# Kernel optimization log

Measured on AMD Instinct MI355X. Metric: run time of the kernel, lower is better.

Reference implementation:

```python
import jax, jax.numpy as jnp
import numpy as np

N_THRESHOLDS = 10


def setup_inputs() -> dict:
    key = jax.random.key(0)
    k1, k2, k3 = jax.random.split(key, 3)
    shape = (32, 1024, 1024)
    prediction = jax.random.normal(k1, shape, dtype=jnp.float32)
    mask = jax.random.randint(k2, shape, 0, 2, dtype=jnp.int32)
    target = jax.random.randint(k3, shape, 0, 2, dtype=jnp.int32)
    return {"prediction": prediction, "mask": mask, "target": target}


def reference(prediction, mask, target):
    # thresholds = linspace(0,1,n+2)[1:-1], same as the torch module
    thresholds = jnp.linspace(0.0, 1.0, N_THRESHOLDS + 2, dtype=jnp.float32)[1:-1]

    s = jax.nn.sigmoid(prediction).ravel()            # [N]
    m = mask.ravel().astype(bool)                     # [N] valid mask
    t = target.ravel().astype(bool)                   # [N]
    mt = m & t                                        # masked positives

    # Broadcast compare against all thresholds at once (single fused pass,
    # no per-threshold host sync like the original loop).
    pos = s[None, :] > thresholds[:, None]            # [T, N] bool

    tp = jnp.sum(pos & mt[None, :], axis=1)           # [T] int32
    p = jnp.sum(pos & m[None, :], axis=1)             # predicted-positive count

    total_m = jnp.sum(m)                              # total valid elements
    total_t = jnp.sum(mt)                             # total true positives in mask

    fp = p - tp
    fn = total_t - tp
    tn = total_m - p - fn

    # classes layout matches torch module: rows = [tp, fp, tn, fn]
    return jnp.stack([tp, fp, tn, fn], axis=0).astype(jnp.float32)
```

## Files before the change

### kernel.cpp

```cpp
#include <hip/hip_runtime.h>


#define NTHR 10
#define NBKT 11
#define NCNT 22
#define WS_STRIDE 16

typedef unsigned long long u64;
typedef unsigned u32;
typedef float __attribute__((ext_vector_type(4))) f32x4;
typedef int   __attribute__((ext_vector_type(4))) i32x4;

__device__ __forceinline__ unsigned wave_reduce_add(unsigned v) {
#pragma unroll
    for (int off = 32; off > 0; off >>= 1)
        v += __shfl_down(v, off, 64);
    return v;
}

__global__ __launch_bounds__(64) void zero_ws_kernel(u32* __restrict__ ws) {
    int i = threadIdx.x;
    if (i < NCNT) ws[i * WS_STRIDE] = 0u;
}

__device__ __forceinline__ void acc_elem(float x, u32 mm, u32 tt, u64& hP, u64& hT) {
    u32 mt = mm & tt;
    float e = __expf(-x);
    float s = __builtin_amdgcn_rcpf(1.0f + e);
    int bi = (int)(s * 11.0f);
    u32 b = (u32)(bi > 10 ? 10 : bi);
    u32 sh = b * 5u;
    hP += (u64)mm << sh;
    hT += (u64)mt << sh;
}

__device__ __forceinline__ void acc_vec(const f32x4& p, const i32x4& m, const i32x4& t,
                                        u64& hP, u64& hT) {
    acc_elem(p.x, (u32)m.x, (u32)t.x, hP, hT);
    acc_elem(p.y, (u32)m.y, (u32)t.y, hP, hT);
    acc_elem(p.z, (u32)m.z, (u32)t.z, hP, hT);
    acc_elem(p.w, (u32)m.w, (u32)t.w, hP, hT);
}

__device__ __forceinline__ void flush_hist(u64& hP, u64& hT,
                                           u64& Plo, u64& Phi, u64& Tlo, u64& Thi) {
#pragma unroll
    for (int b = 0; b < 6; ++b) {
        Plo += (u64)((u32)(hP >> (5 * b)) & 31u) << (10 * b);
        Tlo += (u64)((u32)(hT >> (5 * b)) & 31u) << (10 * b);
    }
#pragma unroll
    for (int b = 6; b < NBKT; ++b) {
        Phi += (u64)((u32)(hP >> (5 * b)) & 31u) << (10 * (b - 6));
        Thi += (u64)((u32)(hT >> (5 * b)) & 31u) << (10 * (b - 6));
    }
    hP = 0ull; hT = 0ull;
}

__global__ __launch_bounds__(256) void count_kernel(
        const f32x4* __restrict__ pred4,
        const i32x4* __restrict__ mask4,
        const i32x4* __restrict__ targ4,
        const float* __restrict__ pred,
        const int*   __restrict__ mask,
        const int*   __restrict__ targ,
        u32* __restrict__ ws, int nvec, int n) {
    u64 Plo = 0ull, Phi = 0ull, Tlo = 0ull, Thi = 0ull;

    const int tid    = blockIdx.x * blockDim.x + threadIdx.x;
    const int lane   = tid & 63;
    const int waveId = tid >> 6;
    const int totalWaves = (gridDim.x * blockDim.x) >> 6;
    const int strideG    = totalWaves << 8;

    for (int base = waveId << 8; base < nvec; base += strideG) {
        u64 hP = 0ull, hT = 0ull;
        if (base + 256 <= nvec) {
            f32x4 p0 = __builtin_nontemporal_load(pred4 + base +       lane);
            f32x4 p1 = __builtin_nontemporal_load(pred4 + base +  64 + lane);
            f32x4 p2 = __builtin_nontemporal_load(pred4 + base + 128 + lane);
            f32x4 p3 = __builtin_nontemporal_load(pred4 + base + 192 + lane);
            i32x4 m0 = __builtin_nontemporal_load(mask4 + base +       lane);
            i32x4 m1 = __builtin_nontemporal_load(mask4 + base +  64 + lane);
            i32x4 m2 = __builtin_nontemporal_load(mask4 + base + 128 + lane);
            i32x4 m3 = __builtin_nontemporal_load(mask4 + base + 192 + lane);
            i32x4 t0 = __builtin_nontemporal_load(targ4 + base +       lane);
            i32x4 t1 = __builtin_nontemporal_load(targ4 + base +  64 + lane);
            i32x4 t2 = __builtin_nontemporal_load(targ4 + base + 128 + lane);
            i32x4 t3 = __builtin_nontemporal_load(targ4 + base + 192 + lane);
            acc_vec(p0, m0, t0, hP, hT);
            acc_vec(p1, m1, t1, hP, hT);
            acc_vec(p2, m2, t2, hP, hT);
            acc_vec(p3, m3, t3, hP, hT);
        } else {
#pragma unroll
            for (int c = 0; c < 4; ++c) {
                int g = base + (c << 6) + lane;
                if (g < nvec) {
                    f32x4 p = __builtin_nontemporal_load(pred4 + g);
                    i32x4 m = __builtin_nontemporal_load(mask4 + g);
                    i32x4 t = __builtin_nontemporal_load(targ4 + g);
                    acc_vec(p, m, t, hP, hT);
                }
            }
        }
        flush_hist(hP, hT, Plo, Phi, Tlo, Thi);
    }

    {
        int i = nvec * 4 + tid;
        if (i < n) {
            u64 hP = 0ull, hT = 0ull;
            acc_elem(pred[i], (u32)mask[i], (u32)targ[i], hP, hT);
            flush_hist(hP, hT, Plo, Phi, Tlo, Thi);
        }
    }

    u32 vals[NCNT];
#pragma unroll
    for (int b = 0; b < 6; ++b) {
        vals[b]        = (u32)(Plo >> (10 * b)) & 1023u;
        vals[NBKT + b] = (u32)(Tlo >> (10 * b)) & 1023u;
    }
#pragma unroll
    for (int b = 6; b < NBKT; ++b) {
        vals[b]        = (u32)(Phi >> (10 * (b - 6))) & 1023u;
        vals[NBKT + b] = (u32)(Thi >> (10 * (b - 6))) & 1023u;
    }
#pragma unroll
    for (int c = 0; c < NCNT; ++c) vals[c] = wave_reduce_add(vals[c]);

    __shared__ u32 partial[4][NCNT];
    const int wave = threadIdx.x >> 6;
    if ((threadIdx.x & 63) == 0) {
#pragma unroll
        for (int c = 0; c < NCNT; ++c) partial[wave][c] = vals[c];
    }
    __syncthreads();
    if (threadIdx.x < NCNT) {
        u32 s = partial[0][threadIdx.x] + partial[1][threadIdx.x] +
                partial[2][threadIdx.x] + partial[3][threadIdx.x];
        atomicAdd(&ws[threadIdx.x * WS_STRIDE], s);
    }
}

__global__ __launch_bounds__(64) void finalize_kernel(const u32* __restrict__ ws,
                                                      float* __restrict__ out) {
    int j = threadIdx.x;
    if (j < NTHR) {
        u32 totM = 0u, totT = 0u, p = 0u, tp = 0u;
#pragma unroll
        for (int b = 0; b < NBKT; ++b) {
            u32 vP = ws[b * WS_STRIDE];
            u32 vT = ws[(NBKT + b) * WS_STRIDE];
            totM += vP; totT += vT;
            if (b > j) { p += vP; tp += vT; }
        }
        u32 fp = p - tp;
        u32 fn = totT - tp;
        u32 tn = totM - p - fn;
        out[j]            = (float)tp;
        out[NTHR + j]     = (float)fp;
        out[2 * NTHR + j] = (float)tn;
        out[3 * NTHR + j] = (float)fn;
    }
}

extern "C" void kernel_launch(void* const* d_in, const int* in_sizes, int n_in,
                              void* d_out, int out_size, void* d_ws, size_t ws_size,
                              hipStream_t stream) {
    const float* pred = (const float*)d_in[0];
    const int*   mask = (const int*)d_in[1];
    const int*   targ = (const int*)d_in[2];
    u32*         ws   = (u32*)d_ws;
    float*       out  = (float*)d_out;

    const int n    = in_sizes[0];
    const int nvec = n / 4;

    zero_ws_kernel<<<1, 64, 0, stream>>>(ws);

    const int blocks = 2048;
    count_kernel<<<blocks, 256, 0, stream>>>(
        (const f32x4*)pred, (const i32x4*)mask, (const i32x4*)targ,
        pred, mask, targ, ws, nvec, n);

    finalize_kernel<<<1, 64, 0, stream>>>(ws, out);
}
```

Before: 332.8 us.

## Double-buffer batch loads in count kernel and halve grid size

```diff
diff --git a/kernel.cpp b/kernel.cpp
--- a/kernel.cpp
+++ b/kernel.cpp
@@ -57,7 +57,66 @@
     hP = 0ull; hT = 0ull;
 }
 
-__global__ __launch_bounds__(256) void count_kernel(
+struct Batch {
+    f32x4 p0, p1, p2, p3;
+    i32x4 m0, m1, m2, m3;
+    i32x4 t0, t1, t2, t3;
+};
+
+__device__ __forceinline__ f32x4 zf4() { f32x4 v; v.x = v.y = v.z = v.w = 0.0f; return v; }
+__device__ __forceinline__ i32x4 zi4() { i32x4 v; v.x = v.y = v.z = v.w = 0;    return v; }
+
+__device__ __forceinline__ void load_batch(Batch& b,
+        const f32x4* __restrict__ pred4, const i32x4* __restrict__ mask4,
+        const i32x4* __restrict__ targ4, int base, int lane, int nvec) {
+    if (base + 256 <= nvec) {
+        b.p0 = __builtin_nontemporal_load(pred4 + base +       lane);
+        b.p1 = __builtin_nontemporal_load(pred4 + base +  64 + lane);
+        b.p2 = __builtin_nontemporal_load(pred4 + base + 128 + lane);
+        b.p3 = __builtin_nontemporal_load(pred4 + base + 192 + lane);
+        b.m0 = __builtin_nontemporal_load(mask4 + base +       lane);
+        b.m1 = __builtin_nontemporal_load(mask4 + base +  64 + lane);
+        b.m2 = __builtin_nontemporal_load(mask4 + base + 128 + lane);
+        b.m3 = __builtin_nontemporal_load(mask4 + base + 192 + lane);
+        b.t0 = __builtin_nontemporal_load(targ4 + base +       lane);
+        b.t1 = __builtin_nontemporal_load(targ4 + base +  64 + lane);
+        b.t2 = __builtin_nontemporal_load(targ4 + base + 128 + lane);
+        b.t3 = __builtin_nontemporal_load(targ4 + base + 192 + lane);
+    } else {
+        int g0 = base +       lane;
+        int g1 = base +  64 + lane;
+        int g2 = base + 128 + lane;
+        int g3 = base + 192 + lane;
+        if (g0 < nvec) { b.p0 = __builtin_nontemporal_load(pred4 + g0);
+                         b.m0 = __builtin_nontemporal_load(mask4 + g0);
+                         b.t0 = __builtin_nontemporal_load(targ4 + g0); }
+        else           { b.p0 = zf4(); b.m0 = zi4(); b.t0 = zi4(); }
+        if (g1 < nvec) { b.p1 = __builtin_nontemporal_load(pred4 + g1);
+                         b.m1 = __builtin_nontemporal_load(mask4 + g1);
+                         b.t1 = __builtin_nontemporal_load(targ4 + g1); }
+        else           { b.p1 = zf4(); b.m1 = zi4(); b.t1 = zi4(); }
+        if (g2 < nvec) { b.p2 = __builtin_nontemporal_load(pred4 + g2);
+                         b.m2 = __builtin_nontemporal_load(mask4 + g2);
+                         b.t2 = __builtin_nontemporal_load(targ4 + g2); }
+        else           { b.p2 = zf4(); b.m2 = zi4(); b.t2 = zi4(); }
+        if (g3 < nvec) { b.p3 = __builtin_nontemporal_load(pred4 + g3);
+                         b.m3 = __builtin_nontemporal_load(mask4 + g3);
+                         b.t3 = __builtin_nontemporal_load(targ4 + g3); }
+        else           { b.p3 = zf4(); b.m3 = zi4(); b.t3 = zi4(); }
+    }
+}
+
+__device__ __forceinline__ void consume_batch(const Batch& b,
+        u64& Plo, u64& Phi, u64& Tlo, u64& Thi) {
+    u64 hP = 0ull, hT = 0ull;
+    acc_vec(b.p0, b.m0, b.t0, hP, hT);
+    acc_vec(b.p1, b.m1, b.t1, hP, hT);
+    acc_vec(b.p2, b.m2, b.t2, hP, hT);
+    acc_vec(b.p3, b.m3, b.t3, hP, hT);
+    flush_hist(hP, hT, Plo, Phi, Tlo, Thi);
+}
+
+__global__ __launch_bounds__(256, 4) void count_kernel(
         const f32x4* __restrict__ pred4,
         const i32x4* __restrict__ mask4,
         const i32x4* __restrict__ targ4,
@@ -73,38 +132,25 @@
     const int totalWaves = (gridDim.x * blockDim.x) >> 6;
     const int strideG    = totalWaves << 8;
 
-    for (int base = waveId << 8; base < nvec; base += strideG) {
-        u64 hP = 0ull, hT = 0ull;
-        if (base + 256 <= nvec) {
-            f32x4 p0 = __builtin_nontemporal_load(pred4 + base +       lane);
-            f32x4 p1 = __builtin_nontemporal_load(pred4 + base +  64 + lane);
-            f32x4 p2 = __builtin_nontemporal_load(pred4 + base + 128 + lane);
-            f32x4 p3 = __builtin_nontemporal_load(pred4 + base + 192 + lane);
-            i32x4 m0 = __builtin_nontemporal_load(mask4 + base +       lane);
-            i32x4 m1 = __builtin_nontemporal_load(mask4 + base +  64 + lane);
-            i32x4 m2 = __builtin_nontemporal_load(mask4 + base + 128 + lane);
-            i32x4 m3 = __builtin_nontemporal_load(mask4 + base + 192 + lane);
-            i32x4 t0 = __builtin_nontemporal_load(targ4 + base +       lane);
-            i32x4 t1 = __builtin_nontemporal_load(targ4 + base +  64 + lane);
-            i32x4 t2 = __builtin_nontemporal_load(targ4 + base + 128 + lane);
-            i32x4 t3 = __builtin_nontemporal_load(targ4 + base + 192 + lane);
-            acc_vec(p0, m0, t0, hP, hT);
-            acc_vec(p1, m1, t1, hP, hT);
-            acc_vec(p2, m2, t2, hP, hT);
-            acc_vec(p3, m3, t3, hP, hT);
-        } else {
-#pragma unroll
-            for (int c = 0; c < 4; ++c) {
-                int g = base + (c << 6) + lane;
-                if (g < nvec) {
-                    f32x4 p = __builtin_nontemporal_load(pred4 + g);
-                    i32x4 m = __builtin_nontemporal_load(mask4 + g);
-                    i32x4 t = __builtin_nontemporal_load(targ4 + g);
-                    acc_vec(p, m, t, hP, hT);
-                }
+    {
+        Batch A, B;
+        int base = waveId << 8;
+        if (base < nvec) {
+            load_batch(A, pred4, mask4, targ4, base, lane, nvec);
+            for (;;) {
+                int nb = base + strideG;
+                if (nb < nvec) load_batch(B, pred4, mask4, targ4, nb, lane, nvec);
+                consume_batch(A, Plo, Phi, Tlo, Thi);
+                if (nb >= nvec) break;
+                base = nb;
+
+                nb = base + strideG;
+                if (nb < nvec) load_batch(A, pred4, mask4, targ4, nb, lane, nvec);
+                consume_batch(B, Plo, Phi, Tlo, Thi);
+                if (nb >= nvec) break;
+                base = nb;
             }
         }
-        flush_hist(hP, hT, Plo, Phi, Tlo, Thi);
     }
 
     {
@@ -180,7 +226,7 @@
 
     zero_ws_kernel<<<1, 64, 0, stream>>>(ws);
 
-    const int blocks = 2048;
+    const int blocks = 1024;
     count_kernel<<<blocks, 256, 0, stream>>>(
         (const f32x4*)pred, (const i32x4*)mask, (const i32x4*)targ,
         pred, mask, targ, ws, nvec, n);
```

New measurement: 422.1 us. 26.8% more time.

## Double-buffer global loads in count kernel and halve grid size

Applied to the files above, without the earlier changes.

```diff
diff --git a/kernel.cpp b/kernel.cpp
--- a/kernel.cpp
+++ b/kernel.cpp
@@ -57,6 +57,56 @@
     hP = 0ull; hT = 0ull;
 }
 
+__device__ __forceinline__ f32x4 zf4() { f32x4 v; v.x = v.y = v.z = v.w = 0.0f; return v; }
+__device__ __forceinline__ i32x4 zi4() { i32x4 v; v.x = v.y = v.z = v.w = 0;    return v; }
+
+#define NTL(p) __builtin_nontemporal_load(p)
+
+#define LOAD_BATCH(S, b)                                                      \
+    do {                                                                      \
+        if ((b) + 256 <= nvec) {                                              \
+            S##p0 = NTL(pred4 + (b) +       lane);                            \
+            S##p1 = NTL(pred4 + (b) +  64 + lane);                            \
+            S##p2 = NTL(pred4 + (b) + 128 + lane);                            \
+            S##p3 = NTL(pred4 + (b) + 192 + lane);                            \
+            S##m0 = NTL(mask4 + (b) +       lane);                            \
+            S##m1 = NTL(mask4 + (b) +  64 + lane);                            \
+            S##m2 = NTL(mask4 + (b) + 128 + lane);                            \
+            S##m3 = NTL(mask4 + (b) + 192 + lane);                            \
+            S##t0 = NTL(targ4 + (b) +       lane);                            \
+            S##t1 = NTL(targ4 + (b) +  64 + lane);                            \
+            S##t2 = NTL(targ4 + (b) + 128 + lane);                            \
+            S##t3 = NTL(targ4 + (b) + 192 + lane);                            \
+        } else {                                                              \
+            int g0 = (b) +       lane;                                        \
+            int g1 = (b) +  64 + lane;                                        \
+            int g2 = (b) + 128 + lane;                                        \
+            int g3 = (b) + 192 + lane;                                        \
+            if (g0 < nvec) { S##p0 = NTL(pred4 + g0); S##m0 = NTL(mask4 + g0);\
+                             S##t0 = NTL(targ4 + g0); }                       \
+            else           { S##p0 = zf4(); S##m0 = zi4(); S##t0 = zi4(); }   \
+            if (g1 < nvec) { S##p1 = NTL(pred4 + g1); S##m1 = NTL(mask4 + g1);\
+                             S##t1 = NTL(targ4 + g1); }                       \
+            else           { S##p1 = zf4(); S##m1 = zi4(); S##t1 = zi4(); }   \
+            if (g2 < nvec) { S##p2 = NTL(pred4 + g2); S##m2 = NTL(mask4 + g2);\
+                             S##t2 = NTL(targ4 + g2); }                       \
+            else           { S##p2 = zf4(); S##m2 = zi4(); S##t2 = zi4(); }   \
+            if (g3 < nvec) { S##p3 = NTL(pred4 + g3); S##m3 = NTL(mask4 + g3);\
+                             S##t3 = NTL(targ4 + g3); }                       \
+            else           { S##p3 = zf4(); S##m3 = zi4(); S##t3 = zi4(); }   \
+        }                                                                     \
+    } while (0)
+
+#define CONSUME_BATCH(S)                                                      \
+    do {                                                                      \
+        u64 hP = 0ull, hT = 0ull;                                             \
+        acc_vec(S##p0, S##m0, S##t0, hP, hT);                                 \
+        acc_vec(S##p1, S##m1, S##t1, hP, hT);                                 \
+        acc_vec(S##p2, S##m2, S##t2, hP, hT);                                 \
+        acc_vec(S##p3, S##m3, S##t3, hP, hT);                                 \
+        flush_hist(hP, hT, Plo, Phi, Tlo, Thi);                               \
+    } while (0)
+
 __global__ __launch_bounds__(256) void count_kernel(
         const f32x4* __restrict__ pred4,
         const i32x4* __restrict__ mask4,
@@ -73,38 +123,30 @@
     const int totalWaves = (gridDim.x * blockDim.x) >> 6;
     const int strideG    = totalWaves << 8;
 
-    for (int base = waveId << 8; base < nvec; base += strideG) {
-        u64 hP = 0ull, hT = 0ull;
-        if (base + 256 <= nvec) {
-            f32x4 p0 = __builtin_nontemporal_load(pred4 + base +       lane);
-            f32x4 p1 = __builtin_nontemporal_load(pred4 + base +  64 + lane);
-            f32x4 p2 = __builtin_nontemporal_load(pred4 + base + 128 + lane);
-            f32x4 p3 = __builtin_nontemporal_load(pred4 + base + 192 + lane);
-            i32x4 m0 = __builtin_nontemporal_load(mask4 + base +       lane);
-            i32x4 m1 = __builtin_nontemporal_load(mask4 + base +  64 + lane);
-            i32x4 m2 = __builtin_nontemporal_load(mask4 + base + 128 + lane);
-            i32x4 m3 = __builtin_nontemporal_load(mask4 + base + 192 + lane);
-            i32x4 t0 = __builtin_nontemporal_load(targ4 + base +       lane);
-            i32x4 t1 = __builtin_nontemporal_load(targ4 + base +  64 + lane);
-            i32x4 t2 = __builtin_nontemporal_load(targ4 + base + 128 + lane);
-            i32x4 t3 = __builtin_nontemporal_load(targ4 + base + 192 + lane);
-            acc_vec(p0, m0, t0, hP, hT);
-            acc_vec(p1, m1, t1, hP, hT);
-            acc_vec(p2, m2, t2, hP, hT);
-            acc_vec(p3, m3, t3, hP, hT);
-        } else {
-#pragma unroll
-            for (int c = 0; c < 4; ++c) {
-                int g = base + (c << 6) + lane;
-                if (g < nvec) {
-                    f32x4 p = __builtin_nontemporal_load(pred4 + g);
-                    i32x4 m = __builtin_nontemporal_load(mask4 + g);
-                    i32x4 t = __builtin_nontemporal_load(targ4 + g);
-                    acc_vec(p, m, t, hP, hT);
-                }
+    {
+        f32x4 Ap0, Ap1, Ap2, Ap3, Bp0, Bp1, Bp2, Bp3;
+        i32x4 Am0, Am1, Am2, Am3, Bm0, Bm1, Bm2, Bm3;
+        i32x4 At0, At1, At2, At3, Bt0, Bt1, Bt2, Bt3;
+
+        int base = waveId << 8;
+        if (base < nvec) {
+            LOAD_BATCH(A, base);
+            for (;;) {
+                int nb = base + strideG;
+                bool more = nb < nvec;
+                if (more) LOAD_BATCH(B, nb);
+                CONSUME_BATCH(A);
+                if (!more) break;
+                base = nb;
+
+                nb = base + strideG;
+                more = nb < nvec;
+                if (more) LOAD_BATCH(A, nb);
+                CONSUME_BATCH(B);
+                if (!more) break;
+                base = nb;
             }
         }
-        flush_hist(hP, hT, Plo, Phi, Tlo, Thi);
     }
 
     {
@@ -180,7 +222,7 @@
 
     zero_ws_kernel<<<1, 64, 0, stream>>>(ws);
 
-    const int blocks = 2048;
+    const int blocks = 1024;
     count_kernel<<<blocks, 256, 0, stream>>>(
         (const f32x4*)pred, (const i32x4*)mask, (const i32x4*)targ,
         pred, mask, targ, ws, nvec, n);
```

New measurement: 330.2 us. Within noise of the previous version (-0.8%).
